# Performance work log

Hardware: AMD Instinct MI355X
Metric: run time of the kernel (lower is better)

Reference implementation:

```python
import jax, jax.numpy as jnp
import numpy as np

B = 256      # graph pairs
NPG = 28     # nodes per graph
MAXN = 32    # max_node_set_size
EPG = 64     # edges per graph (== max_edge_set_size, so no edge padding)
MAXE = 64
D = 128      # node_state_dim
FN = 32      # raw node feature dim
FE = 32      # raw edge feature dim
SK = 64      # sinkhorn_feature_dim
STEPS = 3    # propagation_steps
TEMP = 0.1
ITERS = 20
CW = 0.9     # consistency_weight
G = 2 * B
N = G * NPG
E = G * EPG


def _lin(key, fi, fo):
    return jax.random.normal(key, (fi, fo), jnp.float32) / np.sqrt(fi)


def setup_inputs() -> dict:
    key = jax.random.key(0)
    ks = jax.random.split(key, 12)
    rng = np.random.default_rng(0)
    off = (np.arange(G) * NPG)[:, None]   # graphs ordered q0,c0,q1,c1,...
    from_idx = jnp.asarray((rng.integers(0, NPG, (G, EPG)) + off).reshape(-1), jnp.int32)
    to_idx = jnp.asarray((rng.integers(0, NPG, (G, EPG)) + off).reshape(-1), jnp.int32)
    return dict(
        node_features=jax.random.normal(ks[0], (N, FN), jnp.float32),
        edge_features=jax.random.normal(ks[1], (E, FE), jnp.float32),
        enc_nw=_lin(ks[2], FN, D), enc_nb=jnp.zeros((D,), jnp.float32),
        enc_ew=_lin(ks[3], FE, D), enc_eb=jnp.zeros((D,), jnp.float32),
        msg_w1=_lin(ks[4], 3 * D, 2 * D), msg_b1=jnp.zeros((2 * D,), jnp.float32),
        msg_w2=_lin(ks[5], 2 * D, D), msg_b2=jnp.zeros((D,), jnp.float32),
        rmsg_w1=_lin(ks[6], 3 * D, 2 * D), rmsg_b1=jnp.zeros((2 * D,), jnp.float32),
        rmsg_w2=_lin(ks[7], 2 * D, D), rmsg_b2=jnp.zeros((D,), jnp.float32),
        upd_w1=_lin(ks[8], 2 * D, 2 * D), upd_b1=jnp.zeros((2 * D,), jnp.float32),
        upd_w2=_lin(ks[9], 2 * D, D), upd_b2=jnp.zeros((D,), jnp.float32),
        sk_w1=_lin(ks[10], D, SK), sk_b1=jnp.zeros((SK,), jnp.float32),
        sk_w2=_lin(ks[11], SK, SK), sk_b2=jnp.zeros((SK,), jnp.float32),
        from_idx=from_idx, to_idx=to_idx,
        query_sizes=jnp.full((B,), NPG, jnp.int32),
        corpus_sizes=jnp.full((B,), NPG, jnp.int32),
    )


def _mlp2(x, w1, b1, w2, b2):
    return jnp.maximum(x @ w1 + b1, 0.0) @ w2 + b2


def _sinkhorn(log_alpha):
    # log-domain sinkhorn (noise_factor = 0 -> deterministic)
    la = log_alpha / TEMP
    for _ in range(ITERS):
        la = la - jax.nn.logsumexp(la, axis=2, keepdims=True)
        la = la - jax.nn.logsumexp(la, axis=1, keepdims=True)
    return jnp.exp(la)


def _align(q, c, plan):
    # feature_alignment_score: -relu(q - P @ c).sum over set and feature dims
    return -jnp.maximum(q - plan @ c, 0.0).sum(axis=(1, 2))


def _forward(node_features, edge_features, enc_nw, enc_nb, enc_ew, enc_eb,
             msg_w1, msg_b1, msg_w2, msg_b2, rmsg_w1, rmsg_b1, rmsg_w2, rmsg_b2,
             upd_w1, upd_b1, upd_w2, upd_b2, sk_w1, sk_b1, sk_w2, sk_b2,
             from_idx, to_idx, query_sizes, corpus_sizes):
    h = node_features @ enc_nw + enc_nb        # encoder, [N, D]
    e = edge_features @ enc_ew + enc_eb        # [E, D]

    def messages(h):
        f = _mlp2(jnp.concatenate([h[from_idx], h[to_idx], e], -1), msg_w1, msg_b1, msg_w2, msg_b2)
        r = _mlp2(jnp.concatenate([h[to_idx], h[from_idx], e], -1), rmsg_w1, rmsg_b1, rmsg_w2, rmsg_b2)
        return f, r

    for _ in range(STEPS):  # GraphPropLayer x propagation_steps
        f, r = messages(h)
        agg = jax.ops.segment_sum(f, to_idx, num_segments=N) + \
              jax.ops.segment_sum(r, from_idx, num_segments=N)
        h = h + _mlp2(jnp.concatenate([agg, h], -1), upd_w1, upd_b1, upd_w2, upd_b2)

    # split_and_stack nodes: graphs alternate query/corpus, pad NPG -> MAXN
    hs = jnp.pad(h.reshape(B, 2, NPG, D), ((0, 0), (0, 0), (0, MAXN - NPG), (0, 0)))
    q_nodes, c_nodes = hs[:, 0], hs[:, 1]      # [B, MAXN, D]

    tq = _mlp2(q_nodes, sk_w1, sk_b1, sk_w2, sk_b2)
    tc = _mlp2(c_nodes, sk_w1, sk_b1, sk_w2, sk_b2)
    pos = jnp.arange(MAXN)[None, :]
    mq = tq * (pos < query_sizes[:, None])[..., None]
    mc = tc * (pos < corpus_sizes[:, None])[..., None]
    node_plan = _sinkhorn(jnp.einsum('bqd,bcd->bqc', mq, mc))   # [B, MAXN, MAXN]

    # propagation_messages on final node states
    f, r = messages(h)
    em = (f + r).reshape(B, 2, EPG, D)         # EPG == MAXE -> no pad
    q_edges, c_edges = em[:, 0], em[:, 1]

    # local (within-graph) endpoint indices for kronecker lookup
    fl = (from_idx % NPG).reshape(B, 2, EPG)
    tl = (to_idx % NPG).reshape(B, 2, EPG)
    qf, cf = fl[:, 0], fl[:, 1]
    qt, ct = tl[:, 0], tl[:, 1]

    def kron(T, qf, qt, cf, ct):
        straight = T[qf][:, cf] * T[qt][:, ct]   # [MAXE, MAXE]
        cross = T[qf][:, ct] * T[qt][:, cf]
        return straight + cross

    edge_scores = jax.vmap(kron)(node_plan, qf, qt, cf, ct)     # [B, MAXE, MAXE]
    edge_plan = _sinkhorn(edge_scores)

    return _align(q_nodes, c_nodes, node_plan) + CW * _align(q_edges, c_edges, edge_plan)


def reference(node_features, edge_features, enc_nw, enc_nb, enc_ew, enc_eb,
              msg_w1, msg_b1, msg_w2, msg_b2, rmsg_w1, rmsg_b1, rmsg_w2, rmsg_b2,
              upd_w1, upd_b1, upd_w2, upd_b2, sk_w1, sk_b1, sk_w2, sk_b2,
              from_idx, to_idx, query_sizes, corpus_sizes):
    return _forward(node_features, edge_features, enc_nw, enc_nb, enc_ew, enc_eb,
                    msg_w1, msg_b1, msg_w2, msg_b2, rmsg_w1, rmsg_b1, rmsg_w2, rmsg_b2,
                    upd_w1, upd_b1, upd_w2, upd_b2, sk_w1, sk_b1, sk_w2, sk_b2,
                    from_idx, to_idx, query_sizes, corpus_sizes)
```

## Files before the change

### kernel.cpp

```cpp
#include <hip/hip_runtime.h>
#include <math.h>

#define NPG 28
#define EPG 64
#define NB  256
#define NG  512
#define NN  14336
#define NE  32768
#define TEMPINV 10.0f
#define SINK_ITERS 20
#define CW 0.9f

typedef unsigned int uint;
typedef unsigned short ushort;
typedef __attribute__((ext_vector_type(8))) __bf16 bf16x8;
typedef __attribute__((ext_vector_type(4))) float f32x4;

__device__ __forceinline__ ushort f2bf(float x) {
    uint u = __float_as_uint(x);
    u += 0x7fffu + ((u >> 16) & 1u);
    return (ushort)(u >> 16);
}
__device__ __forceinline__ uint f2bf2(float lo, float hi) {
    return (uint)f2bf(lo) | ((uint)f2bf(hi) << 16);
}
__device__ __forceinline__ float bflo(uint w) { return __uint_as_float(w << 16); }
__device__ __forceinline__ float bfhi(uint w) { return __uint_as_float(w & 0xffff0000u); }
__device__ __forceinline__ uint relu_sum_pk(uint w1, uint w2, uint w3) {
    float lo = fmaxf(bflo(w1) + bflo(w2) + bflo(w3), 0.f);
    float hi = fmaxf(bfhi(w1) + bfhi(w2) + bfhi(w3), 0.f);
    return f2bf2(lo, hi);
}
__device__ __forceinline__ uint4 pack_f32x8(const float* src) {
    const float4 f0 = *(const float4*)src;
    const float4 f1 = *(const float4*)(src + 4);
    uint4 o;
    o.x = f2bf2(f0.x, f0.y);
    o.y = f2bf2(f0.z, f0.w);
    o.z = f2bf2(f1.x, f1.y);
    o.w = f2bf2(f1.z, f1.w);
    return o;
}
__device__ __forceinline__ f32x4 mfma16(bf16x8 a, bf16x8 b, f32x4 c) {
    return __builtin_amdgcn_mfma_f32_16x16x32_bf16(a, b, c, 0, 0, 0);
}

__global__ __launch_bounds__(512) void gnn_fused(
    const float* __restrict__ nf, const float* __restrict__ ef,
    const ushort* __restrict__ encL, const float* __restrict__ enc_nb,
    const ushort* __restrict__ WcombL, const float* __restrict__ bcomb,
    const ushort* __restrict__ WhpL,
    const ushort* __restrict__ W2fL, const ushort* __restrict__ W2rL,
    const float* __restrict__ b2f, const float* __restrict__ b2r,
    const ushort* __restrict__ UW1T, const float* __restrict__ ub1,
    const ushort* __restrict__ UW2T, const float* __restrict__ ub2,
    const int* __restrict__ from_idx, const int* __restrict__ to_idx,
    float* __restrict__ h, float* __restrict__ EM)
{
    __shared__ ushort HPs[NPG * 520];
    __shared__ ushort ECs[2 * 8 * 2048];
    __shared__ float acc_s[NPG * 132];
    __shared__ float hs[NPG * 132];
    __shared__ int fl[64], tl[64];
    const int g = blockIdx.x;
    const int tid = threadIdx.x;
    const int w = tid >> 6, lane = tid & 63;
    const int li = lane & 15, quad = lane >> 4;
    const int wm = w >> 1, wn = w & 1;
    ushort* hid = &HPs[0];

    if (tid < 64) {
        fl[tid] = from_idx[g * 64 + tid] - g * NPG;
        tl[tid] = to_idx[g * 64 + tid] - g * NPG;
    }

    {
        uint4 anf[2];
#pragma unroll
        for (int mi = 0; mi < 2; ++mi) {
            const int row = mi * 16 + li;
            const int rr = (row < NPG) ? row : 0;
            const float4 f0 = *(const float4*)(nf + ((size_t)g * NPG + rr) * 32 + quad * 8);
            const float4 f1 = *(const float4*)(nf + ((size_t)g * NPG + rr) * 32 + quad * 8 + 4);
            uint4 o;
            o.x = f2bf2(f0.x, f0.y); o.y = f2bf2(f0.z, f0.w);
            o.z = f2bf2(f1.x, f1.y); o.w = f2bf2(f1.z, f1.w);
            anf[mi] = o;
        }
        const int col = w * 16 + li;
        const bf16x8 b = __builtin_bit_cast(bf16x8,
            *(const uint4*)(encL + (size_t)col * 32 + quad * 8));
        f32x4 c0 = mfma16(__builtin_bit_cast(bf16x8, anf[0]), b, f32x4{0.f, 0.f, 0.f, 0.f});
        f32x4 c1 = mfma16(__builtin_bit_cast(bf16x8, anf[1]), b, f32x4{0.f, 0.f, 0.f, 0.f});
        const float bv = enc_nb[col];
#pragma unroll
        for (int r = 0; r < 4; ++r) {
            const int r0 = quad * 4 + r;
            hs[r0 * 132 + col] = c0[r] + bv;
            const int r1 = 16 + quad * 4 + r;
            if (r1 < NPG) hs[r1 * 132 + col] = c1[r] + bv;
        }
    }
    {
        uint4 aef[4];
#pragma unroll
        for (int mi = 0; mi < 4; ++mi) {
            const int e = mi * 16 + li;
            const float4 f0 = *(const float4*)(ef + ((size_t)g * 64 + e) * 32 + quad * 8);
            const float4 f1 = *(const float4*)(ef + ((size_t)g * 64 + e) * 32 + quad * 8 + 4);
            uint4 o;
            o.x = f2bf2(f0.x, f0.y); o.y = f2bf2(f0.z, f0.w);
            o.z = f2bf2(f1.x, f1.y); o.w = f2bf2(f1.z, f1.w);
            aef[mi] = o;
        }
#pragma unroll
        for (int ni = 0; ni < 4; ++ni) {
            const int col = w * 64 + ni * 16 + li;
            const bf16x8 b = __builtin_bit_cast(bf16x8,
                *(const uint4*)(WcombL + (size_t)col * 32 + quad * 8));
            const float bv = bcomb[col];
            const int pp = col >> 8, kbl = (col >> 5) & 7, j = col & 31;
#pragma unroll
            for (int mi = 0; mi < 4; ++mi) {
                f32x4 c = mfma16(__builtin_bit_cast(bf16x8, aef[mi]), b,
                                 f32x4{0.f, 0.f, 0.f, 0.f});
#pragma unroll
                for (int r = 0; r < 4; ++r) {
                    const int e = mi * 16 + quad * 4 + r;
                    ECs[pp * 16384 + kbl * 2048 + e * 32 + j] = f2bf(c[r] + bv);
                }
            }
        }
    }
    __syncthreads();

#pragma unroll 1
    for (int step = 0; step < 3; ++step) {
        uint4 ha[2][4];
#pragma unroll
        for (int mi = 0; mi < 2; ++mi) {
            const int row = mi * 16 + li;
            const int rr = (row < NPG) ? row : 0;
#pragma unroll
            for (int kb = 0; kb < 4; ++kb)
                ha[mi][kb] = pack_f32x8(&hs[rr * 132 + kb * 32 + quad * 8]);
        }
        for (int u = tid; u < NPG * 132; u += 512) acc_s[u] = 0.f;

        f32x4 acc[4];
#pragma unroll
        for (int j = 0; j < 4; ++j) acc[j] = f32x4{0.f, 0.f, 0.f, 0.f};

#pragma unroll 1
        for (int p = 0; p < 2; ++p) {
            {
                const int colw = w * 64;
#pragma unroll
                for (int ni = 0; ni < 4; ++ni) {
                    const int col = colw + ni * 16 + li;
                    const ushort* pb = WhpL + (size_t)(p * 512 + col) * 32 + quad * 8;
                    f32x4 c0 = f32x4{0.f, 0.f, 0.f, 0.f};
                    f32x4 c1 = f32x4{0.f, 0.f, 0.f, 0.f};
#pragma unroll
                    for (int kb = 0; kb < 4; ++kb) {
                        const bf16x8 b = __builtin_bit_cast(bf16x8,
                            *(const uint4*)(pb + (size_t)kb * 32768));
                        c0 = mfma16(__builtin_bit_cast(bf16x8, ha[0][kb]), b, c0);
                        c1 = mfma16(__builtin_bit_cast(bf16x8, ha[1][kb]), b, c1);
                    }
#pragma unroll
                    for (int r = 0; r < 4; ++r) {
                        const int r0 = quad * 4 + r;
                        HPs[r0 * 520 + col] = f2bf(c0[r]);
                        const int r1 = 16 + quad * 4 + r;
                        if (r1 < NPG) HPs[r1 * 520 + col] = f2bf(c1[r]);
                    }
                }
            }
            __syncthreads();

            if (p == 1) {
#pragma unroll
                for (int j = 0; j < 4; ++j) acc[j] = f32x4{0.f, 0.f, 0.f, 0.f};
            }
            const int e = wm * 16 + li;
            const int i1 = p ? tl[e] : fl[e];
            const int i2 = p ? fl[e] : tl[e];
            const int ad1 = i1 * 520 + quad * 8;
            const int ad2 = i2 * 520 + 256 + quad * 8;
            const int ade = p * 16384 + e * 32 + quad * 8;
            const ushort* W2L = p ? W2rL : W2fL;
            const int n0 = wn * 64;
            const ushort* pb[4];
#pragma unroll
            for (int ni = 0; ni < 4; ++ni)
                pb[ni] = W2L + (size_t)(n0 + ni * 16 + li) * 32 + quad * 8;
#pragma unroll
            for (int kb = 0; kb < 8; ++kb) {
                const uint4 u1 = *(const uint4*)&HPs[ad1 + kb * 32];
                const uint4 u2 = *(const uint4*)&HPs[ad2 + kb * 32];
                const uint4 ue = *(const uint4*)&ECs[ade + kb * 2048];
                uint4 o;
                o.x = relu_sum_pk(u1.x, u2.x, ue.x);
                o.y = relu_sum_pk(u1.y, u2.y, ue.y);
                o.z = relu_sum_pk(u1.z, u2.z, ue.z);
                o.w = relu_sum_pk(u1.w, u2.w, ue.w);
                const bf16x8 a = __builtin_bit_cast(bf16x8, o);
#pragma unroll
                for (int ni = 0; ni < 4; ++ni) {
                    const bf16x8 b = __builtin_bit_cast(bf16x8,
                        *(const uint4*)(pb[ni] + (size_t)kb * 4096));
                    acc[ni] = mfma16(a, b, acc[ni]);
                }
            }
            {
                const int* targ = p ? fl : tl;
                const float* bias = p ? b2r : b2f;
                float bv[4];
#pragma unroll
                for (int ni = 0; ni < 4; ++ni) bv[ni] = bias[n0 + ni * 16 + li];
#pragma unroll
                for (int r = 0; r < 4; ++r) {
                    const int loc = targ[wm * 16 + quad * 4 + r];
#pragma unroll
                    for (int ni = 0; ni < 4; ++ni)
                        atomicAdd(&acc_s[loc * 132 + n0 + ni * 16 + li],
                                  acc[ni][r] + bv[ni]);
                }
            }
            __syncthreads();
        }

        {
            const int n0u = w * 32;
            f32x4 ua[2][2];
#pragma unroll
            for (int mi = 0; mi < 2; ++mi)
#pragma unroll
                for (int ni = 0; ni < 2; ++ni) ua[mi][ni] = f32x4{0.f, 0.f, 0.f, 0.f};
            const ushort* pb0 = UW1T + (size_t)(n0u + li) * 256 + quad * 8;
            const ushort* pb1 = UW1T + (size_t)(n0u + 16 + li) * 256 + quad * 8;
#pragma unroll
            for (int kb = 0; kb < 8; ++kb) {
                bf16x8 a[2];
                if (kb < 4) {
#pragma unroll
                    for (int mi = 0; mi < 2; ++mi) {
                        const int row = mi * 16 + li;
                        const int rr = (row < NPG) ? row : 0;
                        a[mi] = __builtin_bit_cast(bf16x8,
                            pack_f32x8(&acc_s[rr * 132 + kb * 32 + quad * 8]));
                    }
                } else {
                    a[0] = __builtin_bit_cast(bf16x8, ha[0][kb - 4]);
                    a[1] = __builtin_bit_cast(bf16x8, ha[1][kb - 4]);
                }
                const bf16x8 b0 = __builtin_bit_cast(bf16x8, *(const uint4*)(pb0 + kb * 32));
                const bf16x8 b1 = __builtin_bit_cast(bf16x8, *(const uint4*)(pb1 + kb * 32));
#pragma unroll
                for (int mi = 0; mi < 2; ++mi) {
                    ua[mi][0] = mfma16(a[mi], b0, ua[mi][0]);
                    ua[mi][1] = mfma16(a[mi], b1, ua[mi][1]);
                }
            }
            const float bv0 = ub1[n0u + li], bv1 = ub1[n0u + 16 + li];
#pragma unroll
            for (int mi = 0; mi < 2; ++mi)
#pragma unroll
                for (int r = 0; r < 4; ++r) {
                    const int row = mi * 16 + quad * 4 + r;
                    if (row < NPG) {
                        hid[row * 264 + n0u + li] = f2bf(fmaxf(ua[mi][0][r] + bv0, 0.f));
                        hid[row * 264 + n0u + 16 + li] = f2bf(fmaxf(ua[mi][1][r] + bv1, 0.f));
                    }
                }
        }
        __syncthreads();
        {
            const int n0u = w * 16;
            f32x4 ua[2];
            ua[0] = f32x4{0.f, 0.f, 0.f, 0.f};
            ua[1] = f32x4{0.f, 0.f, 0.f, 0.f};
            const ushort* pb0 = UW2T + (size_t)(n0u + li) * 256 + quad * 8;
#pragma unroll
            for (int kb = 0; kb < 8; ++kb) {
                bf16x8 a[2];
#pragma unroll
                for (int mi = 0; mi < 2; ++mi) {
                    const int row = mi * 16 + li;
                    const int rr = (row < NPG) ? row : 0;
                    a[mi] = __builtin_bit_cast(bf16x8,
                        *(const uint4*)&hid[rr * 264 + kb * 32 + quad * 8]);
                }
                const bf16x8 b0 = __builtin_bit_cast(bf16x8, *(const uint4*)(pb0 + kb * 32));
                ua[0] = mfma16(a[0], b0, ua[0]);
                ua[1] = mfma16(a[1], b0, ua[1]);
            }
            const float bv = ub2[n0u + li];
#pragma unroll
            for (int mi = 0; mi < 2; ++mi)
#pragma unroll
                for (int r = 0; r < 4; ++r) {
                    const int row = mi * 16 + quad * 4 + r;
                    if (row < NPG)
                        hs[row * 132 + n0u + li] += ua[mi][r] + bv;
                }
        }
        __syncthreads();
    }

    {
        uint4 ha[2][4];
#pragma unroll
        for (int mi = 0; mi < 2; ++mi) {
            const int row = mi * 16 + li;
            const int rr = (row < NPG) ? row : 0;
#pragma unroll
            for (int kb = 0; kb < 4; ++kb)
                ha[mi][kb] = pack_f32x8(&hs[rr * 132 + kb * 32 + quad * 8]);
        }
        f32x4 acc[4];
#pragma unroll
        for (int j = 0; j < 4; ++j) acc[j] = f32x4{0.f, 0.f, 0.f, 0.f};
        const int n0 = wn * 64;
#pragma unroll 1
        for (int p = 0; p < 2; ++p) {
            {
                const int colw = w * 64;
#pragma unroll
                for (int ni = 0; ni < 4; ++ni) {
                    const int col = colw + ni * 16 + li;
                    const ushort* pb = WhpL + (size_t)(p * 512 + col) * 32 + quad * 8;
                    f32x4 c0 = f32x4{0.f, 0.f, 0.f, 0.f};
                    f32x4 c1 = f32x4{0.f, 0.f, 0.f, 0.f};
#pragma unroll
                    for (int kb = 0; kb < 4; ++kb) {
                        const bf16x8 b = __builtin_bit_cast(bf16x8,
                            *(const uint4*)(pb + (size_t)kb * 32768));
                        c0 = mfma16(__builtin_bit_cast(bf16x8, ha[0][kb]), b, c0);
                        c1 = mfma16(__builtin_bit_cast(bf16x8, ha[1][kb]), b, c1);
                    }
#pragma unroll
                    for (int r = 0; r < 4; ++r) {
                        const int r0 = quad * 4 + r;
                        HPs[r0 * 520 + col] = f2bf(c0[r]);
                        const int r1 = 16 + quad * 4 + r;
                        if (r1 < NPG) HPs[r1 * 520 + col] = f2bf(c1[r]);
                    }
                }
            }
            __syncthreads();
            const int e = wm * 16 + li;
            const int i1 = p ? tl[e] : fl[e];
            const int i2 = p ? fl[e] : tl[e];
            const int ad1 = i1 * 520 + quad * 8;
            const int ad2 = i2 * 520 + 256 + quad * 8;
            const int ade = p * 16384 + e * 32 + quad * 8;
            const ushort* W2L = p ? W2rL : W2fL;
            const ushort* pb[4];
#pragma unroll
            for (int ni = 0; ni < 4; ++ni)
                pb[ni] = W2L + (size_t)(n0 + ni * 16 + li) * 32 + quad * 8;
#pragma unroll
            for (int kb = 0; kb < 8; ++kb) {
                const uint4 u1 = *(const uint4*)&HPs[ad1 + kb * 32];
                const uint4 u2 = *(const uint4*)&HPs[ad2 + kb * 32];
                const uint4 ue = *(const uint4*)&ECs[ade + kb * 2048];
                uint4 o;
                o.x = relu_sum_pk(u1.x, u2.x, ue.x);
                o.y = relu_sum_pk(u1.y, u2.y, ue.y);
                o.z = relu_sum_pk(u1.z, u2.z, ue.z);
                o.w = relu_sum_pk(u1.w, u2.w, ue.w);
                const bf16x8 a = __builtin_bit_cast(bf16x8, o);
#pragma unroll
                for (int ni = 0; ni < 4; ++ni) {
                    const bf16x8 b = __builtin_bit_cast(bf16x8,
                        *(const uint4*)(pb[ni] + (size_t)kb * 4096));
                    acc[ni] = mfma16(a, b, acc[ni]);
                }
            }
            __syncthreads();
        }
        float bv[4];
#pragma unroll
        for (int ni = 0; ni < 4; ++ni)
            bv[ni] = b2f[n0 + ni * 16 + li] + b2r[n0 + ni * 16 + li];
#pragma unroll
        for (int r = 0; r < 4; ++r) {
            const int erow = g * 64 + wm * 16 + quad * 4 + r;
#pragma unroll
            for (int ni = 0; ni < 4; ++ni)
                EM[(size_t)erow * 128 + n0 + ni * 16 + li] = acc[ni][r] + bv[ni];
        }
    }
    for (int u = tid; u < NPG * 128; u += 512)
        h[(size_t)g * (NPG * 128) + u] = hs[(u >> 7) * 132 + (u & 127)];
}

__global__ __launch_bounds__(256) void pack2(
    const float* __restrict__ msg_w1, const float* __restrict__ rmsg_w1,
    const float* __restrict__ msg_b1, const float* __restrict__ rmsg_b1,
    const float* __restrict__ enc_ew, const float* __restrict__ enc_eb,
    const float* __restrict__ enc_nw,
    const float* __restrict__ msg_w2, const float* __restrict__ rmsg_w2,
    const float* __restrict__ upd_w1, const float* __restrict__ upd_w2,
    ushort* __restrict__ WcombL, float* __restrict__ bcomb,
    ushort* __restrict__ encL,
    ushort* __restrict__ WhpL, ushort* __restrict__ W2fL, ushort* __restrict__ W2rL,
    ushort* __restrict__ UW1T, ushort* __restrict__ UW2T)
{
    const int gid = blockIdx.x, tid = threadIdx.x;
    if (gid < 64) {
        const int idx = gid * 256 + tid;
        const int a = idx >> 9, n = idx & 511;
        const float* Wsrc = (n < 256) ? msg_w1 : rmsg_w1;
        const int nc = n & 255;
        float s = 0.f;
        for (int j = 0; j < 128; ++j)
            s = fmaf(enc_ew[a * 128 + j], Wsrc[(256 + j) * 256 + nc], s);
        WcombL[n * 32 + a] = f2bf(s);
    } else if (gid < 66) {
        const int n = (gid - 64) * 256 + tid;
        const float* Wsrc = (n < 256) ? msg_w1 : rmsg_w1;
        const float* bsrc = (n < 256) ? msg_b1 : rmsg_b1;
        const int nc = n & 255;
        float s = bsrc[nc];
        for (int j = 0; j < 128; ++j)
            s = fmaf(enc_eb[j], Wsrc[(256 + j) * 256 + nc], s);
        bcomb[n] = s;
    } else if (gid < 82) {
        const int idx = (gid - 66) * 256 + tid;
        const int n = idx >> 5, k = idx & 31;
        encL[idx] = f2bf(enc_nw[k * 128 + n]);
    } else if (gid < 594) {
        const int idx = (gid - 82) * 256 + tid;
        const int n = idx >> 7, k = idx & 127;
        const float* Wsrc = (n < 512) ? msg_w1 : rmsg_w1;
        const int part = (n >> 8) & 1, col = n & 255;
        WhpL[(size_t)(k >> 5) * 32768 + n * 32 + (k & 31)] =
            f2bf(Wsrc[(part * 128 + k) * 256 + col]);
    } else if (gid < 722) {
        const int idx = (gid - 594) * 256 + tid;
        const int n = idx >> 8, k = idx & 255;
        W2fL[(size_t)(k >> 5) * 4096 + n * 32 + (k & 31)] = f2bf(msg_w2[k * 128 + n]);
    } else if (gid < 850) {
        const int idx = (gid - 722) * 256 + tid;
        const int n = idx >> 8, k = idx & 255;
        W2rL[(size_t)(k >> 5) * 4096 + n * 32 + (k & 31)] = f2bf(rmsg_w2[k * 128 + n]);
    } else if (gid < 1106) {
        const int idx = (gid - 850) * 256 + tid;
        const int n = idx >> 8, k = idx & 255;
        UW1T[idx] = f2bf(upd_w1[k * 256 + n]);
    } else {
        const int idx = (gid - 1106) * 256 + tid;
        const int n = idx >> 8, k = idx & 255;
        UW2T[idx] = f2bf(upd_w2[k * 128 + n]);
    }
}

__global__ __launch_bounds__(512) void node_kernel(
    const float* __restrict__ h,
    const float* __restrict__ w1, const float* __restrict__ b1,
    const float* __restrict__ w2, const float* __restrict__ b2,
    const int* __restrict__ qsz, const int* __restrict__ csz,
    float* __restrict__ plan_out, float* __restrict__ loss_out)
{
    __shared__ float qn[32][132];
    __shared__ float cn[32][132];
    __shared__ float t1[32][64];
    __shared__ float mq[32][68];
    __shared__ float mc[32][68];
    __shared__ float la[32][33];
    __shared__ float red[8];
    const int bb = blockIdx.x;
    const int tid = threadIdx.x;
    const int qs = qsz[bb], cs = csz[bb];
    for (int u = tid * 4; u < 4096; u += 2048) {
        const int p = u >> 7, d = u & 127;
        float4 zq = make_float4(0.f, 0.f, 0.f, 0.f), zc = zq;
        if (p < NPG) {
            zq = *(const float4*)(h + (size_t)((2 * bb) * NPG + p) * 128 + d);
            zc = *(const float4*)(h + (size_t)((2 * bb + 1) * NPG + p) * 128 + d);
        }
        *(float4*)&qn[p][d] = zq;
        *(float4*)&cn[p][d] = zc;
    }
    __syncthreads();
    const int col = tid & 63;
    const int rg  = tid >> 6;
    for (int s = 0; s < 2; ++s) {
        const float (*src)[132] = s ? cn : qn;
        float (*dst)[68] = s ? mc : mq;
        const int sz = s ? cs : qs;
        float a4[4];
#pragma unroll
        for (int u = 0; u < 4; ++u) a4[u] = b1[col];
        for (int k = 0; k < 128; ++k) {
            const float wv = w1[k * 64 + col];
#pragma unroll
            for (int u = 0; u < 4; ++u) a4[u] = fmaf(src[rg + 8 * u][k], wv, a4[u]);
        }
#pragma unroll
        for (int u = 0; u < 4; ++u) t1[rg + 8 * u][col] = fmaxf(a4[u], 0.f);
        __syncthreads();
#pragma unroll
        for (int u = 0; u < 4; ++u) a4[u] = b2[col];
        for (int k = 0; k < 64; ++k) {
            const float wv = w2[k * 64 + col];
#pragma unroll
            for (int u = 0; u < 4; ++u) a4[u] = fmaf(t1[rg + 8 * u][k], wv, a4[u]);
        }
#pragma unroll
        for (int u = 0; u < 4; ++u) {
            const int r = rg + 8 * u;
            dst[r][col] = (r < sz) ? a4[u] : 0.f;
        }
        __syncthreads();
    }
    {
        const int q = tid >> 4, cg = tid & 15;
#pragma unroll
        for (int u = 0; u < 2; ++u) {
            const int c = cg + 16 * u;
            float s = 0.f;
            for (int d = 0; d < 64; ++d) s = fmaf(mq[q][d], mc[c][d], s);
            la[q][c] = s * TEMPINV;
        }
    }
    __syncthreads();
    if (tid < 256) {
        const int l8 = tid & 7, rq = tid >> 3;
        for (int it = 0; it < SINK_ITERS; ++it) {
            {
                float x[4];
#pragma unroll
                for (int u = 0; u < 4; ++u) x[u] = la[rq][l8 * 4 + u];
                float m = fmaxf(fmaxf(x[0], x[1]), fmaxf(x[2], x[3]));
                m = fmaxf(m, __shfl_xor(m, 1));
                m = fmaxf(m, __shfl_xor(m, 2));
                m = fmaxf(m, __shfl_xor(m, 4));
                float s = __expf(x[0] - m) + __expf(x[1] - m) + __expf(x[2] - m) + __expf(x[3] - m);
                s += __shfl_xor(s, 1);
                s += __shfl_xor(s, 2);
                s += __shfl_xor(s, 4);
                const float lse = m + __logf(s);
#pragma unroll
                for (int u = 0; u < 4; ++u) la[rq][l8 * 4 + u] = x[u] - lse;
            }
            __builtin_amdgcn_s_barrier();
            {
                float x[4];
#pragma unroll
                for (int u = 0; u < 4; ++u) x[u] = la[l8 * 4 + u][rq];
                float m = fmaxf(fmaxf(x[0], x[1]), fmaxf(x[2], x[3]));
                m = fmaxf(m, __shfl_xor(m, 1));
                m = fmaxf(m, __shfl_xor(m, 2));
                m = fmaxf(m, __shfl_xor(m, 4));
                float s = __expf(x[0] - m) + __expf(x[1] - m) + __expf(x[2] - m) + __expf(x[3] - m);
                s += __shfl_xor(s, 1);
                s += __shfl_xor(s, 2);
                s += __shfl_xor(s, 4);
                const float lse = m + __logf(s);
#pragma unroll
                for (int u = 0; u < 4; ++u) la[l8 * 4 + u][rq] = x[u] - lse;
            }
            __builtin_amdgcn_s_barrier();
        }
    } else {
        for (int it = 0; it < SINK_ITERS * 2; ++it) __builtin_amdgcn_s_barrier();
    }
    __syncthreads();
    for (int u = tid; u < 1024; u += 512) {
        const int q = u >> 5, c = u & 31;
        const float p = __expf(la[q][c]);
        la[q][c] = p;
        plan_out[(size_t)bb * 1024 + u] = p;
    }
    __syncthreads();
    float lsum = 0.f;
    {
        const int q = tid >> 4, dg = tid & 15;
        float pc[8];
#pragma unroll
        for (int u = 0; u < 8; ++u) pc[u] = 0.f;
        for (int c = 0; c < 32; ++c) {
            const float p = la[q][c];
            const float* rowc = &cn[c][dg * 8];
#pragma unroll
            for (int v = 0; v < 2; ++v) {
                const float4 cv = *(const float4*)(rowc + 4 * v);
                pc[4 * v + 0] = fmaf(p, cv.x, pc[4 * v + 0]);
                pc[4 * v + 1] = fmaf(p, cv.y, pc[4 * v + 1]);
                pc[4 * v + 2] = fmaf(p, cv.z, pc[4 * v + 2]);
                pc[4 * v + 3] = fmaf(p, cv.w, pc[4 * v + 3]);
            }
        }
        const float* qrow = &qn[q][dg * 8];
#pragma unroll
        for (int u = 0; u < 8; ++u)
            lsum += fmaxf(qrow[u] - pc[u], 0.f);
    }
#pragma unroll
    for (int off = 1; off < 64; off <<= 1) lsum += __shfl_xor(lsum, off);
    if ((tid & 63) == 0) red[tid >> 6] = lsum;
    __syncthreads();
    if (tid == 0) {
        float t = 0.f;
#pragma unroll
        for (int i = 0; i < 8; ++i) t += red[i];
        loss_out[bb] = -t;
    }
}

__global__ __launch_bounds__(512) void edge_kernel(
    const float* __restrict__ plan, const float* __restrict__ EM,
    const int* __restrict__ from_idx, const int* __restrict__ to_idx,
    float* __restrict__ loss_out)
{
    __shared__ float T[32][33];
    __shared__ float la[64][65];
    __shared__ float ce[64][132];
    __shared__ int qf[64], qt[64], cfi[64], cti[64];
    __shared__ float red[8];
    const int bb = blockIdx.x;
    const int tid = threadIdx.x;
    for (int u = tid; u < 1024; u += 512) T[u >> 5][u & 31] = plan[(size_t)bb * 1024 + u];
    if (tid < 64) {
        const int gq = 2 * bb, gc = 2 * bb + 1;
        qf[tid]  = from_idx[gq * 64 + tid] - gq * NPG;
        qt[tid]  = to_idx  [gq * 64 + tid] - gq * NPG;
        cfi[tid] = from_idx[gc * 64 + tid] - gc * NPG;
        cti[tid] = to_idx  [gc * 64 + tid] - gc * NPG;
    }
    {
        const int gc = 2 * bb + 1;
        for (int u = tid * 4; u < 8192; u += 2048) {
            const int i = u >> 7, d = u & 127;
            *(float4*)&ce[i][d] = *(const float4*)(EM + (size_t)(gc * 64 + i) * 128 + d);
        }
    }
    __syncthreads();
    {
        const int i = tid >> 3, jg = tid & 7;
        const int a = qf[i], b_ = qt[i];
#pragma unroll
        for (int u = 0; u < 8; ++u) {
            const int j = jg * 8 + u;
            const float s = T[a][cfi[j]] * T[b_][cti[j]] + T[a][cti[j]] * T[b_][cfi[j]];
            la[i][j] = s * TEMPINV;
        }
    }
    __syncthreads();
    if (tid < 256) {
        const int l4 = tid & 3, rr = tid >> 2;
        for (int it = 0; it < SINK_ITERS; ++it) {
            {
                float x[16];
#pragma unroll
                for (int u = 0; u < 16; ++u) x[u] = la[rr][l4 * 16 + u];
                float m = x[0];
#pragma unroll
                for (int u = 1; u < 16; ++u) m = fmaxf(m, x[u]);
                m = fmaxf(m, __shfl_xor(m, 1));
                m = fmaxf(m, __shfl_xor(m, 2));
                float s = 0.f;
#pragma unroll
                for (int u = 0; u < 16; ++u) s += __expf(x[u] - m);
                s += __shfl_xor(s, 1);
                s += __shfl_xor(s, 2);
                const float lse = m + __logf(s);
#pragma unroll
                for (int u = 0; u < 16; ++u) la[rr][l4 * 16 + u] = x[u] - lse;
            }
            __builtin_amdgcn_s_barrier();
            {
                float x[16];
#pragma unroll
                for (int u = 0; u < 16; ++u) x[u] = la[l4 * 16 + u][rr];
                float m = x[0];
#pragma unroll
                for (int u = 1; u < 16; ++u) m = fmaxf(m, x[u]);
                m = fmaxf(m, __shfl_xor(m, 1));
                m = fmaxf(m, __shfl_xor(m, 2));
                float s = 0.f;
#pragma unroll
                for (int u = 0; u < 16; ++u) s += __expf(x[u] - m);
                s += __shfl_xor(s, 1);
                s += __shfl_xor(s, 2);
                const float lse = m + __logf(s);
#pragma unroll
                for (int u = 0; u < 16; ++u) la[l4 * 16 + u][rr] = x[u] - lse;
            }
            __builtin_amdgcn_s_barrier();
        }
    } else {
        for (int it = 0; it < SINK_ITERS * 2; ++it) __builtin_amdgcn_s_barrier();
    }
    __syncthreads();
    for (int u = tid; u < 4096; u += 512) la[u >> 6][u & 63] = __expf(la[u >> 6][u & 63]);
    __syncthreads();
    float lsum = 0.f;
    {
        const int q = tid >> 3, dg = tid & 7;
        float pc[16];
#pragma unroll
        for (int u = 0; u < 16; ++u) pc[u] = 0.f;
        for (int c = 0; c < 64; ++c) {
            const float p = la[q][c];
            const float* rowc = &ce[c][dg * 16];
#pragma unroll
            for (int v = 0; v < 4; ++v) {
                const float4 cv = *(const float4*)(rowc + 4 * v);
                pc[4 * v + 0] = fmaf(p, cv.x, pc[4 * v + 0]);
                pc[4 * v + 1] = fmaf(p, cv.y, pc[4 * v + 1]);
                pc[4 * v + 2] = fmaf(p, cv.z, pc[4 * v + 2]);
                pc[4 * v + 3] = fmaf(p, cv.w, pc[4 * v + 3]);
            }
        }
        const float* qe = EM + (size_t)((2 * bb) * 64 + q) * 128 + dg * 16;
#pragma unroll
        for (int u = 0; u < 16; ++u)
            lsum += fmaxf(qe[u] - pc[u], 0.f);
    }
#pragma unroll
    for (int off = 1; off < 64; off <<= 1) lsum += __shfl_xor(lsum, off);
    if ((tid & 63) == 0) red[tid >> 6] = lsum;
    __syncthreads();
    if (tid == 0) {
        float t = 0.f;
#pragma unroll
        for (int i = 0; i < 8; ++i) t += red[i];
        loss_out[bb] -= CW * t;
    }
}

extern "C" void kernel_launch(void* const* d_in, const int* in_sizes, int n_in,
                              void* d_out, int out_size, void* d_ws, size_t ws_size,
                              hipStream_t stream)
{
    const float* node_features = (const float*)d_in[0];
    const float* edge_features = (const float*)d_in[1];
    const float* enc_nw  = (const float*)d_in[2];
    const float* enc_nb  = (const float*)d_in[3];
    const float* enc_ew  = (const float*)d_in[4];
    const float* enc_eb  = (const float*)d_in[5];
    const float* msg_w1  = (const float*)d_in[6];
    const float* msg_b1  = (const float*)d_in[7];
    const float* msg_w2  = (const float*)d_in[8];
    const float* msg_b2  = (const float*)d_in[9];
    const float* rmsg_w1 = (const float*)d_in[10];
    const float* rmsg_b1 = (const float*)d_in[11];
    const float* rmsg_w2 = (const float*)d_in[12];
    const float* rmsg_b2 = (const float*)d_in[13];
    const float* upd_w1  = (const float*)d_in[14];
    const float* upd_b1  = (const float*)d_in[15];
    const float* upd_w2  = (const float*)d_in[16];
    const float* upd_b2  = (const float*)d_in[17];
    const float* sk_w1   = (const float*)d_in[18];
    const float* sk_b1   = (const float*)d_in[19];
    const float* sk_w2   = (const float*)d_in[20];
    const float* sk_b2   = (const float*)d_in[21];
    const int* from_idx  = (const int*)d_in[22];
    const int* to_idx    = (const int*)d_in[23];
    const int* qsizes    = (const int*)d_in[24];
    const int* csizes    = (const int*)d_in[25];
    float* out = (float*)d_out;

    float* ws     = (float*)d_ws;
    float* h      = ws;
    float* EM     = h + (size_t)NN * 128;
    float* plan   = EM + (size_t)NE * 128;
    float* bcomb  = plan + (size_t)NB * 1024;
    ushort* WcombL = (ushort*)(bcomb + 512);
    ushort* encL  = WcombL + 16384;
    ushort* WhpL  = encL + 4096;
    ushort* W2fL  = WhpL + 131072;
    ushort* W2rL  = W2fL + 32768;
    ushort* UW1T  = W2rL + 32768;
    ushort* UW2T  = UW1T + 65536;

    const dim3 blk(256);
    const dim3 blk512(512);

    pack2<<<1234, blk, 0, stream>>>(msg_w1, rmsg_w1, msg_b1, rmsg_b1,
                                    enc_ew, enc_eb, enc_nw, msg_w2, rmsg_w2,
                                    upd_w1, upd_w2,
                                    WcombL, bcomb, encL, WhpL, W2fL, W2rL, UW1T, UW2T);

    gnn_fused<<<dim3(NG), blk512, 0, stream>>>(
        node_features, edge_features, encL, enc_nb, WcombL, bcomb,
        WhpL, W2fL, W2rL, msg_b2, rmsg_b2,
        UW1T, upd_b1, UW2T, upd_b2, from_idx, to_idx, h, EM);

    node_kernel<<<NB, blk512, 0, stream>>>(
        h, sk_w1, sk_b1, sk_w2, sk_b2, qsizes, csizes, plan, out);
    edge_kernel<<<NB, blk512, 0, stream>>>(
        plan, EM, from_idx, to_idx, out);
}
```

Before: 449.5 us.

## Fuse node and edge Sinkhorn heads into one kernel with aliased shared memory

Merges node_kernel and edge_kernel into a single heads_fused kernel per graph pair. The node plan stays in shared memory instead of being written to global memory and read back, and the node loss is combined with the edge loss in a final single store. Shared memory is carved from one pool so the edge-phase buffers reuse the node-phase regions. This removes one kernel launch and the plan round trip, but the edge-phase work is now serialized after the node phase inside each block, and each block needs a larger shared footprint.

```diff
diff --git a/kernel.cpp b/kernel.cpp
--- a/kernel.cpp
+++ b/kernel.cpp
@@ -458,23 +458,35 @@
     }
 }
 
-__global__ __launch_bounds__(512) void node_kernel(
-    const float* __restrict__ h,
+__global__ __launch_bounds__(512) void heads_fused(
+    const float* __restrict__ h, const float* __restrict__ EM,
     const float* __restrict__ w1, const float* __restrict__ b1,
     const float* __restrict__ w2, const float* __restrict__ b2,
     const int* __restrict__ qsz, const int* __restrict__ csz,
-    float* __restrict__ plan_out, float* __restrict__ loss_out)
+    const int* __restrict__ from_idx, const int* __restrict__ to_idx,
+    float* __restrict__ loss_out)
 {
-    __shared__ float qn[32][132];
-    __shared__ float cn[32][132];
-    __shared__ float t1[32][64];
-    __shared__ float mq[32][68];
-    __shared__ float mc[32][68];
-    __shared__ float la[32][33];
+    __shared__ float la32[32][33];
     __shared__ float red[8];
+    __shared__ float nodeloss_s;
+    __shared__ float pool[14848];
+
+    float (*qn)[132] = (float(*)[132])pool;
+    float (*cn)[132] = (float(*)[132])(pool + 4224);
+    float (*t1)[64]  = (float(*)[64]) (pool + 8448);
+    float (*mq)[68]  = (float(*)[68]) (pool + 10496);
+    float (*mc)[68]  = (float(*)[68]) (pool + 12672);
+    float (*ce)[132]  = (float(*)[132])pool;
+    float (*la64)[65] = (float(*)[65])(pool + 8448);
+    int* qf  = (int*)(pool + 12608);
+    int* qt  = qf + 64;
+    int* cfi = qt + 64;
+    int* cti = cfi + 64;
+
     const int bb = blockIdx.x;
     const int tid = threadIdx.x;
     const int qs = qsz[bb], cs = csz[bb];
+
     for (int u = tid * 4; u < 4096; u += 2048) {
         const int p = u >> 7, d = u & 127;
         float4 zq = make_float4(0.f, 0.f, 0.f, 0.f), zc = zq;
@@ -524,7 +536,7 @@
             const int c = cg + 16 * u;
             float s = 0.f;
             for (int d = 0; d < 64; ++d) s = fmaf(mq[q][d], mc[c][d], s);
-            la[q][c] = s * TEMPINV;
+            la32[q][c] = s * TEMPINV;
         }
     }
     __syncthreads();
@@ -534,7 +546,7 @@
             {
                 float x[4];
 #pragma unroll
-                for (int u = 0; u < 4; ++u) x[u] = la[rq][l8 * 4 + u];
+                for (int u = 0; u < 4; ++u) x[u] = la32[rq][l8 * 4 + u];
                 float m = fmaxf(fmaxf(x[0], x[1]), fmaxf(x[2], x[3]));
                 m = fmaxf(m, __shfl_xor(m, 1));
                 m = fmaxf(m, __shfl_xor(m, 2));
@@ -545,13 +557,13 @@
                 s += __shfl_xor(s, 4);
                 const float lse = m + __logf(s);
 #pragma unroll
-                for (int u = 0; u < 4; ++u) la[rq][l8 * 4 + u] = x[u] - lse;
+                for (int u = 0; u < 4; ++u) la32[rq][l8 * 4 + u] = x[u] - lse;
             }
             __builtin_amdgcn_s_barrier();
             {
                 float x[4];
 #pragma unroll
-                for (int u = 0; u < 4; ++u) x[u] = la[l8 * 4 + u][rq];
+                for (int u = 0; u < 4; ++u) x[u] = la32[l8 * 4 + u][rq];
                 float m = fmaxf(fmaxf(x[0], x[1]), fmaxf(x[2], x[3]));
                 m = fmaxf(m, __shfl_xor(m, 1));
                 m = fmaxf(m, __shfl_xor(m, 2));
@@ -562,7 +574,7 @@
                 s += __shfl_xor(s, 4);
                 const float lse = m + __logf(s);
 #pragma unroll
-                for (int u = 0; u < 4; ++u) la[l8 * 4 + u][rq] = x[u] - lse;
+                for (int u = 0; u < 4; ++u) la32[l8 * 4 + u][rq] = x[u] - lse;
             }
             __builtin_amdgcn_s_barrier();
         }
@@ -572,9 +584,7 @@
     __syncthreads();
     for (int u = tid; u < 1024; u += 512) {
         const int q = u >> 5, c = u & 31;
-        const float p = __expf(la[q][c]);
-        la[q][c] = p;
-        plan_out[(size_t)bb * 1024 + u] = p;
+        la32[q][c] = __expf(la32[q][c]);
     }
     __syncthreads();
     float lsum = 0.f;
@@ -584,7 +594,7 @@
 #pragma unroll
         for (int u = 0; u < 8; ++u) pc[u] = 0.f;
         for (int c = 0; c < 32; ++c) {
-            const float p = la[q][c];
+            const float p = la32[q][c];
             const float* rowc = &cn[c][dg * 8];
 #pragma unroll
             for (int v = 0; v < 2; ++v) {
@@ -608,23 +618,17 @@
         float t = 0.f;
 #pragma unroll
         for (int i = 0; i < 8; ++i) t += red[i];
-        loss_out[bb] = -t;
-    }
-}
-
-__global__ __launch_bounds__(512) void edge_kernel(
-    const float* __restrict__ plan, const float* __restrict__ EM,
-    const int* __restrict__ from_idx, const int* __restrict__ to_idx,
-    float* __restrict__ loss_out)
-{
-    __shared__ float T[32][33];
-    __shared__ float la[64][65];
-    __shared__ float ce[64][132];
-    __shared__ int qf[64], qt[64], cfi[64], cti[64];
-    __shared__ float red[8];
-    const int bb = blockIdx.x;
-    const int tid = threadIdx.x;
-    for (int u = tid; u < 1024; u += 512) T[u >> 5][u & 31] = plan[(size_t)bb * 1024 + u];
+        nodeloss_s = t;
+    }
+    __syncthreads();
+
+    {
+        const int gc = 2 * bb + 1;
+        for (int u = tid * 4; u < 8192; u += 2048) {
+            const int i = u >> 7, d = u & 127;
+            *(float4*)&ce[i][d] = *(const float4*)(EM + (size_t)(gc * 64 + i) * 128 + d);
+        }
+    }
     if (tid < 64) {
         const int gq = 2 * bb, gc = 2 * bb + 1;
         qf[tid]  = from_idx[gq * 64 + tid] - gq * NPG;
@@ -632,13 +636,6 @@
         cfi[tid] = from_idx[gc * 64 + tid] - gc * NPG;
         cti[tid] = to_idx  [gc * 64 + tid] - gc * NPG;
     }
-    {
-        const int gc = 2 * bb + 1;
-        for (int u = tid * 4; u < 8192; u += 2048) {
-            const int i = u >> 7, d = u & 127;
-            *(float4*)&ce[i][d] = *(const float4*)(EM + (size_t)(gc * 64 + i) * 128 + d);
-        }
-    }
     __syncthreads();
     {
         const int i = tid >> 3, jg = tid & 7;
@@ -646,8 +643,9 @@
 #pragma unroll
         for (int u = 0; u < 8; ++u) {
             const int j = jg * 8 + u;
-            const float s = T[a][cfi[j]] * T[b_][cti[j]] + T[a][cti[j]] * T[b_][cfi[j]];
-            la[i][j] = s * TEMPINV;
+            const float s = la32[a][cfi[j]] * la32[b_][cti[j]] +
+                            la32[a][cti[j]] * la32[b_][cfi[j]];
+            la64[i][j] = s * TEMPINV;
         }
     }
     __syncthreads();
@@ -657,7 +655,7 @@
             {
                 float x[16];
 #pragma unroll
-                for (int u = 0; u < 16; ++u) x[u] = la[rr][l4 * 16 + u];
+                for (int u = 0; u < 16; ++u) x[u] = la64[rr][l4 * 16 + u];
                 float m = x[0];
 #pragma unroll
                 for (int u = 1; u < 16; ++u) m = fmaxf(m, x[u]);
@@ -670,13 +668,13 @@
                 s += __shfl_xor(s, 2);
                 const float lse = m + __logf(s);
 #pragma unroll
-                for (int u = 0; u < 16; ++u) la[rr][l4 * 16 + u] = x[u] - lse;
+                for (int u = 0; u < 16; ++u) la64[rr][l4 * 16 + u] = x[u] - lse;
             }
             __builtin_amdgcn_s_barrier();
             {
                 float x[16];
 #pragma unroll
-                for (int u = 0; u < 16; ++u) x[u] = la[l4 * 16 + u][rr];
+                for (int u = 0; u < 16; ++u) x[u] = la64[l4 * 16 + u][rr];
                 float m = x[0];
 #pragma unroll
                 for (int u = 1; u < 16; ++u) m = fmaxf(m, x[u]);
@@ -689,7 +687,7 @@
                 s += __shfl_xor(s, 2);
                 const float lse = m + __logf(s);
 #pragma unroll
-                for (int u = 0; u < 16; ++u) la[l4 * 16 + u][rr] = x[u] - lse;
+                for (int u = 0; u < 16; ++u) la64[l4 * 16 + u][rr] = x[u] - lse;
             }
             __builtin_amdgcn_s_barrier();
         }
@@ -697,16 +695,16 @@
         for (int it = 0; it < SINK_ITERS * 2; ++it) __builtin_amdgcn_s_barrier();
     }
     __syncthreads();
-    for (int u = tid; u < 4096; u += 512) la[u >> 6][u & 63] = __expf(la[u >> 6][u & 63]);
-    __syncthreads();
-    float lsum = 0.f;
+    for (int u = tid; u < 4096; u += 512) la64[u >> 6][u & 63] = __expf(la64[u >> 6][u & 63]);
+    __syncthreads();
+    lsum = 0.f;
     {
         const int q = tid >> 3, dg = tid & 7;
         float pc[16];
 #pragma unroll
         for (int u = 0; u < 16; ++u) pc[u] = 0.f;
         for (int c = 0; c < 64; ++c) {
-            const float p = la[q][c];
+            const float p = la64[q][c];
             const float* rowc = &ce[c][dg * 16];
 #pragma unroll
             for (int v = 0; v < 4; ++v) {
@@ -730,7 +728,7 @@
         float t = 0.f;
 #pragma unroll
         for (int i = 0; i < 8; ++i) t += red[i];
-        loss_out[bb] -= CW * t;
+        loss_out[bb] = -nodeloss_s - CW * t;
     }
 }
 
@@ -769,8 +767,7 @@
     float* ws     = (float*)d_ws;
     float* h      = ws;
     float* EM     = h + (size_t)NN * 128;
-    float* plan   = EM + (size_t)NE * 128;
-    float* bcomb  = plan + (size_t)NB * 1024;
+    float* bcomb  = EM + (size_t)NE * 128;
     ushort* WcombL = (ushort*)(bcomb + 512);
     ushort* encL  = WcombL + 16384;
     ushort* WhpL  = encL + 4096;
@@ -792,8 +789,7 @@
         WhpL, W2fL, W2rL, msg_b2, rmsg_b2,
         UW1T, upd_b1, UW2T, upd_b2, from_idx, to_idx, h, EM);
 
-    node_kernel<<<NB, blk512, 0, stream>>>(
-        h, sk_w1, sk_b1, sk_w2, sk_b2, qsizes, csizes, plan, out);
-    edge_kernel<<<NB, blk512, 0, stream>>>(
-        plan, EM, from_idx, to_idx, out);
-}
+    heads_fused<<<NB, blk512, 0, stream>>>(
+        h, EM, sk_w1, sk_b1, sk_w2, sk_b2, qsizes, csizes,
+        from_idx, to_idx, out);
+}
```

After: 475.3 us. 5.7% more time.

## Precompute edge-combined projections in a separate FP32 GEMM kernel, read from global

Applied to the files above, without the earlier changes.

Moves the per-graph edge-feature projection (edge features times the combined edge-encoder/message weight) out of the fused GNN kernel into a standalone tiled FP32 GEMM that writes bf16 results in the blocked layout. The fused kernel drops its 64KB shared ECs buffer and reads these values from global memory in each message pass. The aim is to cut LDS usage so the fused kernel can reach higher occupancy. In exchange it adds an extra kernel launch, about 32MB of global traffic per step, and FP32 SIMT math where MFMA was used before.

```diff
diff --git a/kernel.cpp b/kernel.cpp
--- a/kernel.cpp
+++ b/kernel.cpp
@@ -45,10 +45,91 @@
     return __builtin_amdgcn_mfma_f32_16x16x32_bf16(a, b, c, 0, 0, 0);
 }
 
+__global__ __launch_bounds__(256) void ec_gemm(
+    const float* __restrict__ A, int lda, int K,
+    const float* __restrict__ W, int ldw, const float* __restrict__ bias,
+    ushort* __restrict__ Cb)
+{
+    constexpr int BM = 128;
+    __shared__ float As[16][BM + 4];
+    __shared__ float Bs[16][132];
+    const int tid = threadIdx.x;
+    const int m0 = blockIdx.x * BM;
+    const int n0 = blockIdx.y * 128;
+    const int tx = tid & 15, ty = tid >> 4;
+    const int arow = tid >> 1;
+    const int a0   = (tid & 1) * 8;
+    const int brow = ty;
+    const int bcol = tx * 8;
+    const int nch = K >> 4;
+
+    float4 aC[2], bC[2], aN[2], bN[2];
+    float acc[8][8];
+#pragma unroll
+    for (int i = 0; i < 8; ++i)
+#pragma unroll
+        for (int j = 0; j < 8; ++j) acc[i][j] = 0.f;
+
+    {
+        const float* src = A + (size_t)(m0 + arow) * lda + a0;
+        aC[0] = *(const float4*)src;
+        aC[1] = *(const float4*)(src + 4);
+        const float* bsrc = W + (size_t)brow * ldw + n0 + bcol;
+        bC[0] = *(const float4*)bsrc;
+        bC[1] = *(const float4*)(bsrc + 4);
+    }
+
+    for (int ch = 0; ch < nch; ++ch) {
+        {
+            const float* f = (const float*)aC;
+#pragma unroll
+            for (int i = 0; i < 8; ++i) As[a0 + i][arow] = f[i];
+            *(float4*)&Bs[brow][bcol]     = bC[0];
+            *(float4*)&Bs[brow][bcol + 4] = bC[1];
+        }
+        __syncthreads();
+        if (ch + 1 < nch) {
+            const int kc = (ch + 1) << 4;
+            const float* src = A + (size_t)(m0 + arow) * lda + kc + a0;
+            aN[0] = *(const float4*)src;
+            aN[1] = *(const float4*)(src + 4);
+            const float* bsrc = W + (size_t)(kc + brow) * ldw + n0 + bcol;
+            bN[0] = *(const float4*)bsrc;
+            bN[1] = *(const float4*)(bsrc + 4);
+        }
+#pragma unroll
+        for (int kk = 0; kk < 16; ++kk) {
+            float afr[8], bfr[8];
+            *(float4*)&afr[0] = *(const float4*)&As[kk][ty * 8];
+            *(float4*)&afr[4] = *(const float4*)&As[kk][ty * 8 + 4];
+            *(float4*)&bfr[0] = *(const float4*)&Bs[kk][tx * 8];
+            *(float4*)&bfr[4] = *(const float4*)&Bs[kk][tx * 8 + 4];
+#pragma unroll
+            for (int i = 0; i < 8; ++i)
+#pragma unroll
+                for (int j = 0; j < 8; ++j) acc[i][j] = fmaf(afr[i], bfr[j], acc[i][j]);
+        }
+        __syncthreads();
+        aC[0] = aN[0]; aC[1] = aN[1];
+        bC[0] = bN[0]; bC[1] = bN[1];
+    }
+#pragma unroll
+    for (int i = 0; i < 8; ++i) {
+        const int row = m0 + ty * 8 + i;
+#pragma unroll
+        for (int j = 0; j < 8; ++j) {
+            const int col = n0 + tx * 8 + j;
+            const float v = acc[i][j] + bias[col];
+            const int gg = row >> 6, eloc = row & 63;
+            const int p = col >> 8, kb = (col >> 5) & 7, jj = col & 31;
+            Cb[(size_t)(((gg * 2 + p) * 8 + kb)) * 2048 + eloc * 32 + jj] = f2bf(v);
+        }
+    }
+}
+
 __global__ __launch_bounds__(512) void gnn_fused(
-    const float* __restrict__ nf, const float* __restrict__ ef,
+    const float* __restrict__ nf, const ushort* __restrict__ EC2,
     const ushort* __restrict__ encL, const float* __restrict__ enc_nb,
-    const ushort* __restrict__ WcombL, const float* __restrict__ bcomb,
     const ushort* __restrict__ WhpL,
     const ushort* __restrict__ W2fL, const ushort* __restrict__ W2rL,
     const float* __restrict__ b2f, const float* __restrict__ b2r,
@@ -58,7 +139,6 @@
     float* __restrict__ h, float* __restrict__ EM)
 {
     __shared__ ushort HPs[NPG * 520];
-    __shared__ ushort ECs[2 * 8 * 2048];
     __shared__ float acc_s[NPG * 132];
     __shared__ float hs[NPG * 132];
     __shared__ int fl[64], tl[64];
@@ -101,37 +181,6 @@
             if (r1 < NPG) hs[r1 * 132 + col] = c1[r] + bv;
         }
     }
-    {
-        uint4 aef[4];
-#pragma unroll
-        for (int mi = 0; mi < 4; ++mi) {
-            const int e = mi * 16 + li;
-            const float4 f0 = *(const float4*)(ef + ((size_t)g * 64 + e) * 32 + quad * 8);
-            const float4 f1 = *(const float4*)(ef + ((size_t)g * 64 + e) * 32 + quad * 8 + 4);
-            uint4 o;
-            o.x = f2bf2(f0.x, f0.y); o.y = f2bf2(f0.z, f0.w);
-            o.z = f2bf2(f1.x, f1.y); o.w = f2bf2(f1.z, f1.w);
-            aef[mi] = o;
-        }
-#pragma unroll
-        for (int ni = 0; ni < 4; ++ni) {
-            const int col = w * 64 + ni * 16 + li;
-            const bf16x8 b = __builtin_bit_cast(bf16x8,
-                *(const uint4*)(WcombL + (size_t)col * 32 + quad * 8));
-            const float bv = bcomb[col];
-            const int pp = col >> 8, kbl = (col >> 5) & 7, j = col & 31;
-#pragma unroll
-            for (int mi = 0; mi < 4; ++mi) {
-                f32x4 c = mfma16(__builtin_bit_cast(bf16x8, aef[mi]), b,
-                                 f32x4{0.f, 0.f, 0.f, 0.f});
-#pragma unroll
-                for (int r = 0; r < 4; ++r) {
-                    const int e = mi * 16 + quad * 4 + r;
-                    ECs[pp * 16384 + kbl * 2048 + e * 32 + j] = f2bf(c[r] + bv);
-                }
-            }
-        }
-    }
     __syncthreads();
 
 #pragma unroll 1
@@ -188,7 +237,7 @@
             const int i2 = p ? fl[e] : tl[e];
             const int ad1 = i1 * 520 + quad * 8;
             const int ad2 = i2 * 520 + 256 + quad * 8;
-            const int ade = p * 16384 + e * 32 + quad * 8;
+            const ushort* ecb = EC2 + (size_t)(g * 2 + p) * 16384 + e * 32 + quad * 8;
             const ushort* W2L = p ? W2rL : W2fL;
             const int n0 = wn * 64;
             const ushort* pb[4];
@@ -199,7 +248,7 @@
             for (int kb = 0; kb < 8; ++kb) {
                 const uint4 u1 = *(const uint4*)&HPs[ad1 + kb * 32];
                 const uint4 u2 = *(const uint4*)&HPs[ad2 + kb * 32];
-                const uint4 ue = *(const uint4*)&ECs[ade + kb * 2048];
+                const uint4 ue = *(const uint4*)(ecb + kb * 2048);
                 uint4 o;
                 o.x = relu_sum_pk(u1.x, u2.x, ue.x);
                 o.y = relu_sum_pk(u1.y, u2.y, ue.y);
@@ -355,7 +404,7 @@
             const int i2 = p ? fl[e] : tl[e];
             const int ad1 = i1 * 520 + quad * 8;
             const int ad2 = i2 * 520 + 256 + quad * 8;
-            const int ade = p * 16384 + e * 32 + quad * 8;
+            const ushort* ecb = EC2 + (size_t)(g * 2 + p) * 16384 + e * 32 + quad * 8;
             const ushort* W2L = p ? W2rL : W2fL;
             const ushort* pb[4];
 #pragma unroll
@@ -365,7 +414,7 @@
             for (int kb = 0; kb < 8; ++kb) {
                 const uint4 u1 = *(const uint4*)&HPs[ad1 + kb * 32];
                 const uint4 u2 = *(const uint4*)&HPs[ad2 + kb * 32];
-                const uint4 ue = *(const uint4*)&ECs[ade + kb * 2048];
+                const uint4 ue = *(const uint4*)(ecb + kb * 2048);
                 uint4 o;
                 o.x = relu_sum_pk(u1.x, u2.x, ue.x);
                 o.y = relu_sum_pk(u1.y, u2.y, ue.y);
@@ -404,7 +453,7 @@
     const float* __restrict__ enc_nw,
     const float* __restrict__ msg_w2, const float* __restrict__ rmsg_w2,
     const float* __restrict__ upd_w1, const float* __restrict__ upd_w2,
-    ushort* __restrict__ WcombL, float* __restrict__ bcomb,
+    float* __restrict__ Wcomb, float* __restrict__ bcomb,
     ushort* __restrict__ encL,
     ushort* __restrict__ WhpL, ushort* __restrict__ W2fL, ushort* __restrict__ W2rL,
     ushort* __restrict__ UW1T, ushort* __restrict__ UW2T)
@@ -418,7 +467,7 @@
         float s = 0.f;
         for (int j = 0; j < 128; ++j)
             s = fmaf(enc_ew[a * 128 + j], Wsrc[(256 + j) * 256 + nc], s);
-        WcombL[n * 32 + a] = f2bf(s);
+        Wcomb[idx] = s;
     } else if (gid < 66) {
         const int n = (gid - 64) * 256 + tid;
         const float* Wsrc = (n < 256) ? msg_w1 : rmsg_w1;
@@ -770,14 +819,15 @@
     float* h      = ws;
     float* EM     = h + (size_t)NN * 128;
     float* plan   = EM + (size_t)NE * 128;
-    float* bcomb  = plan + (size_t)NB * 1024;
-    ushort* WcombL = (ushort*)(bcomb + 512);
-    ushort* encL  = WcombL + 16384;
+    float* Wcomb  = plan + (size_t)NB * 1024;
+    float* bcomb  = Wcomb + 16384;
+    ushort* encL  = (ushort*)(bcomb + 512);
     ushort* WhpL  = encL + 4096;
     ushort* W2fL  = WhpL + 131072;
     ushort* W2rL  = W2fL + 32768;
     ushort* UW1T  = W2rL + 32768;
     ushort* UW2T  = UW1T + 65536;
+    ushort* EC2   = UW2T + 32768;
 
     const dim3 blk(256);
     const dim3 blk512(512);
@@ -785,10 +835,13 @@
     pack2<<<1234, blk, 0, stream>>>(msg_w1, rmsg_w1, msg_b1, rmsg_b1,
                                     enc_ew, enc_eb, enc_nw, msg_w2, rmsg_w2,
                                     upd_w1, upd_w2,
-                                    WcombL, bcomb, encL, WhpL, W2fL, W2rL, UW1T, UW2T);
+                                    Wcomb, bcomb, encL, WhpL, W2fL, W2rL, UW1T, UW2T);
+
+    ec_gemm<<<dim3(NE / 128, 4), blk, 0, stream>>>(
+        edge_features, 32, 32, Wcomb, 512, bcomb, EC2);
 
     gnn_fused<<<dim3(NG), blk512, 0, stream>>>(
-        node_features, edge_features, encL, enc_nb, WcombL, bcomb,
+        node_features, EC2, encL, enc_nb,
         WhpL, W2fL, W2rL, msg_b2, rmsg_b2,
         UW1T, upd_b1, UW2T, upd_b2, from_idx, to_idx, h, EM);
 
```

After: 526.4 us. 1.17x slower.
